# Performance work log

Hardware: AMD Instinct MI355X
Metric: run time of the kernel (lower is better)

The kernel has to match this reference:

```python
import jax, jax.numpy as jnp
import numpy as np

B, T, N_EMBED, HEAD_SIZE = 4096, 50, 600, 100
CHUNK = N_EMBED // HEAD_SIZE  # 6: per-group input channels of the grouped 1x1 conv


def _grouped_proj(x, w):
    # Conv1d(kernel=1, groups=HEAD_SIZE, bias=False): output channel h is a dot
    # product of its weight row with the h-th CHUNK-slice of the embedding.
    xr = x.reshape(x.shape[0], x.shape[1], HEAD_SIZE, CHUNK)  # [B,T,H,chunk]
    return jnp.einsum('bthc,hc->bth', xr, w)  # [B,T,HEAD_SIZE]


def setup_inputs() -> dict:
    key = jax.random.key(0)
    k0, k1, k2, k3 = jax.random.split(key, 4)
    scale = 1.0 / np.sqrt(CHUNK)
    x = jax.random.normal(k0, (B, T, N_EMBED), dtype=jnp.float32)
    w_q = jax.random.normal(k1, (HEAD_SIZE, CHUNK), dtype=jnp.float32) * scale
    w_k = jax.random.normal(k2, (HEAD_SIZE, CHUNK), dtype=jnp.float32) * scale
    w_v = jax.random.normal(k3, (HEAD_SIZE, CHUNK), dtype=jnp.float32) * scale
    return {"x": x, "w_q": w_q, "w_k": w_k, "w_v": w_v}


def reference(x, w_q, w_k, w_v):
    Bx, Tx, C = x.shape
    q = _grouped_proj(x, w_q)  # [B,T,H]
    k = _grouped_proj(x, w_k)  # [B,T,H]
    v = _grouped_proj(x, w_v)  # [B,T,H]
    # scores scaled by full embed dim C (as in the source), causal mask, softmax
    wei = jnp.einsum('bth,bsh->bts', q, k) * (C ** -0.5)  # [B,T,T]
    causal = jnp.tril(jnp.ones((Tx, Tx), dtype=bool))
    wei = jnp.where(causal, wei, -jnp.inf)
    wei = jax.nn.softmax(wei, axis=-1)
    out = jnp.einsum('bts,bsh->bth', wei, v)  # [B,T,HEAD_SIZE]
    return out
```

## Files before the change

kernel.cpp:

```cpp
#include <hip/hip_runtime.h>
#include <hip/hip_bf16.h>


#define BATCH 4096
#define TT 50
#define HH 100
#define CC 600

typedef __attribute__((ext_vector_type(8))) short short8;
typedef __attribute__((ext_vector_type(4))) short short4v;
typedef __attribute__((ext_vector_type(4))) float f32x4;
typedef unsigned short ushort_t;

constexpr int NTHR = 256;
constexpr int NWAVES = 4;
constexpr float kScale = 0.04082482904638630163f;

constexpr int OQ = 0, OKk = 6400, OV = 12800, OP = 19968, LDS_US = 24064;

__device__ __forceinline__ ushort_t f2bf(float f) {
    return __builtin_bit_cast(ushort_t, __float2bfloat16(f));
}
__device__ __forceinline__ float bf2f(ushort_t h) {
    return __uint_as_float(((unsigned)h) << 16);
}

__global__ __launch_bounds__(NTHR, 3) void headc_fused(
    const float* __restrict__ x,
    const float* __restrict__ wq,
    const float* __restrict__ wk,
    const float* __restrict__ wv,
    float* __restrict__ out)
{
    __shared__ __align__(16) ushort_t lds[LDS_US];

    const int b = blockIdx.x;
    const int tid = threadIdx.x;
    const float* xb = x + (size_t)b * (TT * CC);

    {
        const short8 z8 = {0, 0, 0, 0, 0, 0, 0, 0};
        const short4v z4 = {0, 0, 0, 0};
        if (tid < 100) {
            const int arr = tid / 50;
            const int r = tid % 50;
            const int base = (arr ? OKk : OQ) + r * 128;
            *reinterpret_cast<short4v*>(lds + base + ((12 ^ (r & 7)) << 3) + 4) = z4;
            *reinterpret_cast<short8*>(lds + base + ((13 ^ (r & 7)) << 3)) = z8;
            *reinterpret_cast<short8*>(lds + base + ((14 ^ (r & 7)) << 3)) = z8;
            *reinterpret_cast<short8*>(lds + base + ((15 ^ (r & 7)) << 3)) = z8;
            #pragma unroll
            for (int rr = 0; rr < 2; ++rr) {
                const int vr = tid + rr * 100;
                if (vr < 100) {
                    *reinterpret_cast<short4v*>(lds + OV + vr * 64 + ((6 ^ (vr & 7)) << 3) + 4) = z4;
                    *reinterpret_cast<short8*>(lds + OV + vr * 64 + ((7 ^ (vr & 7)) << 3)) = z8;
                }
            }
        } else if (tid < 196) {
            const int idx = tid - 100;
            const int r = 100 + (idx >> 3);
            const int gr = idx & 7;
            *reinterpret_cast<short8*>(lds + OV + r * 64 + gr * 8) = z8;
        } else if (tid < 246) {
            const int vr = tid - 196 + 50;
            *reinterpret_cast<short4v*>(lds + OV + vr * 64 + ((6 ^ (vr & 7)) << 3) + 4) = z4;
            *reinterpret_cast<short8*>(lds + OV + vr * 64 + ((7 ^ (vr & 7)) << 3)) = z8;
        }
    }

    if (tid < 250) {
        const int hp = tid % 50;
        const int c  = tid / 50;
        const int h0 = hp * 2;
        const float4 wqa = *(const float4*)(wq + h0 * 6);
        const float4 wqb = *(const float4*)(wq + h0 * 6 + 4);
        const float4 wqc = *(const float4*)(wq + h0 * 6 + 8);
        const float4 wka = *(const float4*)(wk + h0 * 6);
        const float4 wkb = *(const float4*)(wk + h0 * 6 + 4);
        const float4 wkc = *(const float4*)(wk + h0 * 6 + 8);
        const float4 wva = *(const float4*)(wv + h0 * 6);
        const float4 wvb = *(const float4*)(wv + h0 * 6 + 4);
        const float4 wvc = *(const float4*)(wv + h0 * 6 + 8);

        #pragma unroll
        for (int u = 0; u < 3; ++u) {
            const int qd = c + u * 5;
            if (qd <= 12) {
                const int tbase = qd * 4;
                float4 xr[4][3];
                #pragma unroll
                for (int r = 0; r < 4; ++r) {
                    const int tc = (tbase + r < TT) ? (tbase + r) : (TT - 1);
                    const float* xp = xb + tc * CC + h0 * 6;
                    xr[r][0] = *(const float4*)xp;
                    xr[r][1] = *(const float4*)(xp + 4);
                    xr[r][2] = *(const float4*)(xp + 8);
                }
                short4v vp0 = {0, 0, 0, 0};
                short4v vp1 = {0, 0, 0, 0};
                #pragma unroll
                for (int r = 0; r < 4; ++r) {
                    const int t = tbase + r;
                    const float4 xa = xr[r][0], xm = xr[r][1], xc = xr[r][2];
                    float q0 = xa.x*wqa.x + xa.y*wqa.y + xa.z*wqa.z + xa.w*wqa.w + xm.x*wqb.x + xm.y*wqb.y;
                    float q1 = xm.z*wqb.z + xm.w*wqb.w + xc.x*wqc.x + xc.y*wqc.y + xc.z*wqc.z + xc.w*wqc.w;
                    float k0 = xa.x*wka.x + xa.y*wka.y + xa.z*wka.z + xa.w*wka.w + xm.x*wkb.x + xm.y*wkb.y;
                    float k1 = xm.z*wkb.z + xm.w*wkb.w + xc.x*wkc.x + xc.y*wkc.y + xc.z*wkc.z + xc.w*wkc.w;
                    float v0 = xa.x*wva.x + xa.y*wva.y + xa.z*wva.z + xa.w*wva.w + xm.x*wvb.x + xm.y*wvb.y;
                    float v1 = xm.z*wvb.z + xm.w*wvb.w + xc.x*wvc.x + xc.y*wvc.y + xc.z*wvc.z + xc.w*wvc.w;
                    q0 *= kScale; q1 *= kScale;
                    if (t < TT) {
                        const int qg = (((h0 >> 3) ^ (t & 7)) << 3) + (h0 & 7);
                        *reinterpret_cast<unsigned*>(lds + OQ  + t * 128 + qg) =
                            (unsigned)f2bf(q0) | ((unsigned)f2bf(q1) << 16);
                        *reinterpret_cast<unsigned*>(lds + OKk + t * 128 + qg) =
                            (unsigned)f2bf(k0) | ((unsigned)f2bf(k1) << 16);
                        vp0[r] = (short)f2bf(v0);
                        vp1[r] = (short)f2bf(v1);
                    }
                }
                const int g = qd >> 1, half = (qd & 1) * 4;
                *reinterpret_cast<short4v*>(lds + OV + h0 * 64 + ((g ^ (h0 & 7)) << 3) + half) = vp0;
                *reinterpret_cast<short4v*>(lds + OV + (h0 + 1) * 64 + ((g ^ ((h0 + 1) & 7)) << 3) + half) = vp1;
            }
        }
    }
    __syncthreads();

    const int wv_ = tid >> 6;
    const int lane = tid & 63;
    const int l15 = lane & 15, l4 = lane >> 4;

    for (int p = wv_; p < 10; p += NWAVES) {
        const int tm = (p >= 6) ? 3 : (p >= 3) ? 2 : (p >= 1) ? 1 : 0;
        const int sn = p - tm * (tm + 1) / 2;
        f32x4 acc = {0.f, 0.f, 0.f, 0.f};
        const int ar = tm * 16 + l15;
        const int br = sn * 16 + l15;
        #pragma unroll
        for (int kk = 0; kk < 4; ++kk) {
            const int g = kk * 4 + l4;
            const short8 a  = *reinterpret_cast<const short8*>(lds + OQ  + ar * 128 + ((g ^ (ar & 7)) << 3));
            const short8 bb = *reinterpret_cast<const short8*>(lds + OKk + br * 128 + ((g ^ (br & 7)) << 3));
            acc = __builtin_amdgcn_mfma_f32_16x16x32_bf16(a, bb, acc, 0, 0, 0);
        }
        const int row0 = tm * 16 + l4 * 4;
        const int col = sn * 16 + l15;
        #pragma unroll
        for (int r = 0; r < 4; ++r) {
            const int row = row0 + r;
            lds[OP + row * 64 + (((col >> 3) ^ (row & 7)) << 3) + (col & 7)] = f2bf(acc[r]);
        }
    }
    __syncthreads();

    {
        const int t = tid >> 2, ll = tid & 3;
        if (t < TT) {
            const int ga = (2 * ll) ^ (t & 7), gb = (2 * ll + 1) ^ (t & 7);
            const short8 pa = *reinterpret_cast<const short8*>(lds + OP + t * 64 + (ga << 3));
            const short8 pb = *reinterpret_cast<const short8*>(lds + OP + t * 64 + (gb << 3));
            float v[16];
            float mx = -3.4e38f;
            #pragma unroll
            for (int j = 0; j < 8; ++j) {
                const int s = 16 * ll + j;
                v[j] = bf2f((ushort_t)pa[j]);
                if (s <= t) mx = fmaxf(mx, v[j]);
            }
            #pragma unroll
            for (int j = 0; j < 8; ++j) {
                const int s = 16 * ll + 8 + j;
                v[8 + j] = bf2f((ushort_t)pb[j]);
                if (s <= t) mx = fmaxf(mx, v[8 + j]);
            }
            mx = fmaxf(mx, __shfl_xor(mx, 1));
            mx = fmaxf(mx, __shfl_xor(mx, 2));
            float sum = 0.f;
            #pragma unroll
            for (int j = 0; j < 16; ++j) {
                const int s = 16 * ll + j;
                const float e = (s <= t) ? __expf(v[j] - mx) : 0.f;
                v[j] = e;
                sum += e;
            }
            sum += __shfl_xor(sum, 1);
            sum += __shfl_xor(sum, 2);
            const float inv = 1.f / sum;
            short8 wa, wb;
            #pragma unroll
            for (int j = 0; j < 8; ++j) {
                wa[j] = (short)f2bf(v[j] * inv);
                wb[j] = (short)f2bf(v[8 + j] * inv);
            }
            *reinterpret_cast<short8*>(lds + OP + t * 64 + (ga << 3)) = wa;
            *reinterpret_cast<short8*>(lds + OP + t * 64 + (gb << 3)) = wb;
        }
    }
    __syncthreads();

    float* ob = out + (size_t)b * (TT * HH);
    for (int p = wv_; p < 28; p += NWAVES) {
        const int tm = p / 7, hn = p - tm * 7;
        f32x4 acc = {0.f, 0.f, 0.f, 0.f};
        const int ar = tm * 16 + l15;
        const int br = hn * 16 + l15;
        #pragma unroll
        for (int kk = 0; kk < 2; ++kk) {
            const int g = kk * 4 + l4;
            const short8 a  = *reinterpret_cast<const short8*>(lds + OP + ar * 64 + ((g ^ (ar & 7)) << 3));
            const short8 bb = *reinterpret_cast<const short8*>(lds + OV + br * 64 + ((g ^ (br & 7)) << 3));
            acc = __builtin_amdgcn_mfma_f32_16x16x32_bf16(a, bb, acc, 0, 0, 0);
        }
        const int h = hn * 16 + l15;
        const int t0 = tm * 16 + l4 * 4;
        if (h < HH) {
            #pragma unroll
            for (int r = 0; r < 4; ++r) {
                const int t = t0 + r;
                if (t < TT) ob[t * HH + h] = acc[r];
            }
        }
    }
}

extern "C" void kernel_launch(void* const* d_in, const int* in_sizes, int n_in,
                              void* d_out, int out_size, void* d_ws, size_t ws_size,
                              hipStream_t stream) {
    const float* x  = (const float*)d_in[0];
    const float* wq = (const float*)d_in[1];
    const float* wk = (const float*)d_in[2];
    const float* wv = (const float*)d_in[3];
    float* out = (float*)d_out;
    headc_fused<<<dim3(BATCH), dim3(NTHR), 0, stream>>>(x, wq, wk, wv, out);
}
```

Measured before the change: 121.5 us.

## Process eight batches per block with double-buffered LDS and prefetched x loads

Each block now handles eight batch elements in sequence instead of one. The x loads for the next element are issued into registers before the current element's attention runs, and the projection writes into an alternate LDS buffer, so global-memory latency overlaps with MFMA and softmax work. The score matrix P reuses the other buffer's Q region. This raises register use (three x tile sets held at once) and LDS per block, lowers occupancy to two blocks per SM in launch bounds, and leaves a grid of only 512 blocks, which may not fill the device well.

```diff
diff --git a/kernel.cpp b/kernel.cpp
--- a/kernel.cpp
+++ b/kernel.cpp
@@ -14,9 +14,14 @@
 
 constexpr int NTHR = 256;
 constexpr int NWAVES = 4;
+constexpr int NB = 8;
+constexpr int GRID = BATCH / NB;
 constexpr float kScale = 0.04082482904638630163f;
 
-constexpr int OQ = 0, OKk = 6400, OV = 12800, OP = 19968, LDS_US = 24064;
+constexpr int BUF_US = 19200;
+constexpr int RQ = 0, RK = 6400, RV = 12800;
+constexpr int PAD_US = 38400;
+constexpr int LDS_US = 39168;
 
 __device__ __forceinline__ ushort_t f2bf(float f) {
     return __builtin_bit_cast(ushort_t, __float2bfloat16(f));
@@ -24,8 +29,13 @@
 __device__ __forceinline__ float bf2f(ushort_t h) {
     return __uint_as_float(((unsigned)h) << 16);
 }
-
-__global__ __launch_bounds__(NTHR, 3) void headc_fused(
+__device__ __forceinline__ void bar_lds() {
+    asm volatile("s_waitcnt lgkmcnt(0)" ::: "memory");
+    __builtin_amdgcn_s_barrier();
+    asm volatile("" ::: "memory");
+}
+
+__global__ __launch_bounds__(NTHR, 2) void headc_fused(
     const float* __restrict__ x,
     const float* __restrict__ wq,
     const float* __restrict__ wk,
@@ -34,193 +44,232 @@
 {
     __shared__ __align__(16) ushort_t lds[LDS_US];
 
-    const int b = blockIdx.x;
     const int tid = threadIdx.x;
-    const float* xb = x + (size_t)b * (TT * CC);
+    const float* xblk = x + (size_t)blockIdx.x * NB * (TT * CC);
+    float* oblk = out + (size_t)blockIdx.x * NB * (TT * HH);
+
+    const int hp = tid % 50;
+    const int c = tid / 50;
+    const int h0 = hp * 2;
+    const int nqd = (c >= 3) ? 2 : 3;
+    const bool pactive = (tid < 250);
 
     {
         const short8 z8 = {0, 0, 0, 0, 0, 0, 0, 0};
         const short4v z4 = {0, 0, 0, 0};
-        if (tid < 100) {
-            const int arr = tid / 50;
-            const int r = tid % 50;
-            const int base = (arr ? OKk : OQ) + r * 128;
-            *reinterpret_cast<short4v*>(lds + base + ((12 ^ (r & 7)) << 3) + 4) = z4;
-            *reinterpret_cast<short8*>(lds + base + ((13 ^ (r & 7)) << 3)) = z8;
-            *reinterpret_cast<short8*>(lds + base + ((14 ^ (r & 7)) << 3)) = z8;
-            *reinterpret_cast<short8*>(lds + base + ((15 ^ (r & 7)) << 3)) = z8;
-            #pragma unroll
-            for (int rr = 0; rr < 2; ++rr) {
-                const int vr = tid + rr * 100;
-                if (vr < 100) {
-                    *reinterpret_cast<short4v*>(lds + OV + vr * 64 + ((6 ^ (vr & 7)) << 3) + 4) = z4;
-                    *reinterpret_cast<short8*>(lds + OV + vr * 64 + ((7 ^ (vr & 7)) << 3)) = z8;
-                }
-            }
-        } else if (tid < 196) {
-            const int idx = tid - 100;
-            const int r = 100 + (idx >> 3);
-            const int gr = idx & 7;
-            *reinterpret_cast<short8*>(lds + OV + r * 64 + gr * 8) = z8;
-        } else if (tid < 246) {
-            const int vr = tid - 196 + 50;
-            *reinterpret_cast<short4v*>(lds + OV + vr * 64 + ((6 ^ (vr & 7)) << 3) + 4) = z4;
-            *reinterpret_cast<short8*>(lds + OV + vr * 64 + ((7 ^ (vr & 7)) << 3)) = z8;
-        }
+        for (int j = tid; j < 400; j += NTHR) {
+            if (j < 200) {
+                const int buf = (j >= 100) ? BUF_US : 0;
+                const int arr = ((j / 50) & 1) ? RK : RQ;
+                const int r = j % 50;
+                const int base = buf + arr + r * 128;
+                *reinterpret_cast<short4v*>(lds + base + ((12 ^ (r & 7)) << 3) + 4) = z4;
+                *reinterpret_cast<short8*>(lds + base + ((13 ^ (r & 7)) << 3)) = z8;
+                *reinterpret_cast<short8*>(lds + base + ((14 ^ (r & 7)) << 3)) = z8;
+                *reinterpret_cast<short8*>(lds + base + ((15 ^ (r & 7)) << 3)) = z8;
+            } else {
+                const int jj = j - 200;
+                const int buf = (jj >= 100) ? BUF_US : 0;
+                const int h = jj % 100;
+                const int base = buf + RV + h * 64;
+                *reinterpret_cast<short4v*>(lds + base + ((6 ^ (h & 7)) << 3) + 4) = z4;
+                *reinterpret_cast<short8*>(lds + base + ((7 ^ (h & 7)) << 3)) = z8;
+            }
+        }
+        for (int j = tid; j < 96; j += NTHR)
+            *reinterpret_cast<short8*>(lds + PAD_US + j * 8) = z8;
     }
 
-    if (tid < 250) {
-        const int hp = tid % 50;
-        const int c  = tid / 50;
-        const int h0 = hp * 2;
-        const float4 wqa = *(const float4*)(wq + h0 * 6);
-        const float4 wqb = *(const float4*)(wq + h0 * 6 + 4);
-        const float4 wqc = *(const float4*)(wq + h0 * 6 + 8);
-        const float4 wka = *(const float4*)(wk + h0 * 6);
-        const float4 wkb = *(const float4*)(wk + h0 * 6 + 4);
-        const float4 wkc = *(const float4*)(wk + h0 * 6 + 8);
-        const float4 wva = *(const float4*)(wv + h0 * 6);
-        const float4 wvb = *(const float4*)(wv + h0 * 6 + 4);
-        const float4 wvc = *(const float4*)(wv + h0 * 6 + 8);
-
-        #pragma unroll
-        for (int u = 0; u < 3; ++u) {
-            const int qd = c + u * 5;
-            if (qd <= 12) {
-                const int tbase = qd * 4;
-                float4 xr[4][3];
-                #pragma unroll
-                for (int r = 0; r < 4; ++r) {
-                    const int tc = (tbase + r < TT) ? (tbase + r) : (TT - 1);
-                    const float* xp = xb + tc * CC + h0 * 6;
-                    xr[r][0] = *(const float4*)xp;
-                    xr[r][1] = *(const float4*)(xp + 4);
-                    xr[r][2] = *(const float4*)(xp + 8);
-                }
-                short4v vp0 = {0, 0, 0, 0};
-                short4v vp1 = {0, 0, 0, 0};
-                #pragma unroll
-                for (int r = 0; r < 4; ++r) {
-                    const int t = tbase + r;
-                    const float4 xa = xr[r][0], xm = xr[r][1], xc = xr[r][2];
-                    float q0 = xa.x*wqa.x + xa.y*wqa.y + xa.z*wqa.z + xa.w*wqa.w + xm.x*wqb.x + xm.y*wqb.y;
-                    float q1 = xm.z*wqb.z + xm.w*wqb.w + xc.x*wqc.x + xc.y*wqc.y + xc.z*wqc.z + xc.w*wqc.w;
-                    float k0 = xa.x*wka.x + xa.y*wka.y + xa.z*wka.z + xa.w*wka.w + xm.x*wkb.x + xm.y*wkb.y;
-                    float k1 = xm.z*wkb.z + xm.w*wkb.w + xc.x*wkc.x + xc.y*wkc.y + xc.z*wkc.z + xc.w*wkc.w;
-                    float v0 = xa.x*wva.x + xa.y*wva.y + xa.z*wva.z + xa.w*wva.w + xm.x*wvb.x + xm.y*wvb.y;
-                    float v1 = xm.z*wvb.z + xm.w*wvb.w + xc.x*wvc.x + xc.y*wvc.y + xc.z*wvc.z + xc.w*wvc.w;
-                    q0 *= kScale; q1 *= kScale;
-                    if (t < TT) {
-                        const int qg = (((h0 >> 3) ^ (t & 7)) << 3) + (h0 & 7);
-                        *reinterpret_cast<unsigned*>(lds + OQ  + t * 128 + qg) =
-                            (unsigned)f2bf(q0) | ((unsigned)f2bf(q1) << 16);
-                        *reinterpret_cast<unsigned*>(lds + OKk + t * 128 + qg) =
-                            (unsigned)f2bf(k0) | ((unsigned)f2bf(k1) << 16);
-                        vp0[r] = (short)f2bf(v0);
-                        vp1[r] = (short)f2bf(v1);
+    float4 w0, w1, w2, w3, w4, w5, w6, w7, w8;
+    if (pactive) {
+        w0 = *(const float4*)(wq + h0 * 6);
+        w1 = *(const float4*)(wq + h0 * 6 + 4);
+        w2 = *(const float4*)(wq + h0 * 6 + 8);
+        w3 = *(const float4*)(wk + h0 * 6);
+        w4 = *(const float4*)(wk + h0 * 6 + 4);
+        w5 = *(const float4*)(wk + h0 * 6 + 8);
+        w6 = *(const float4*)(wv + h0 * 6);
+        w7 = *(const float4*)(wv + h0 * 6 + 4);
+        w8 = *(const float4*)(wv + h0 * 6 + 8);
+    }
+
+    float4 xr[3][4][3];
+
+    auto issue_x = [&](int bi) {
+        if (pactive) {
+            const float* xb = xblk + (size_t)bi * (TT * CC);
+            #pragma unroll
+            for (int u = 0; u < 3; ++u) {
+                if (u < nqd) {
+                    const int tb = (c + u * 5) * 4;
+                    #pragma unroll
+                    for (int r = 0; r < 4; ++r) {
+                        const int tc = (tb + r < TT) ? (tb + r) : (TT - 1);
+                        const float* xp = xb + tc * CC + h0 * 6;
+                        xr[u][r][0] = *(const float4*)xp;
+                        xr[u][r][1] = *(const float4*)(xp + 4);
+                        xr[u][r][2] = *(const float4*)(xp + 8);
                     }
                 }
-                const int g = qd >> 1, half = (qd & 1) * 4;
-                *reinterpret_cast<short4v*>(lds + OV + h0 * 64 + ((g ^ (h0 & 7)) << 3) + half) = vp0;
-                *reinterpret_cast<short4v*>(lds + OV + (h0 + 1) * 64 + ((g ^ ((h0 + 1) & 7)) << 3) + half) = vp1;
-            }
-        }
-    }
-    __syncthreads();
+            }
+        }
+    };
+
+    auto do_proj = [&](int base) {
+        if (pactive) {
+            #pragma unroll
+            for (int u = 0; u < 3; ++u) {
+                if (u < nqd) {
+                    const int qd = c + u * 5;
+                    const int tb = qd * 4;
+                    short4v vp0 = {0, 0, 0, 0}, vp1 = {0, 0, 0, 0};
+                    #pragma unroll
+                    for (int r = 0; r < 4; ++r) {
+                        const int t = tb + r;
+                        const float4 xa = xr[u][r][0], xm = xr[u][r][1], xc = xr[u][r][2];
+                        float q0 = xa.x*w0.x + xa.y*w0.y + xa.z*w0.z + xa.w*w0.w + xm.x*w1.x + xm.y*w1.y;
+                        float q1 = xm.z*w1.z + xm.w*w1.w + xc.x*w2.x + xc.y*w2.y + xc.z*w2.z + xc.w*w2.w;
+                        float k0 = xa.x*w3.x + xa.y*w3.y + xa.z*w3.z + xa.w*w3.w + xm.x*w4.x + xm.y*w4.y;
+                        float k1 = xm.z*w4.z + xm.w*w4.w + xc.x*w5.x + xc.y*w5.y + xc.z*w5.z + xc.w*w5.w;
+                        float v0 = xa.x*w6.x + xa.y*w6.y + xa.z*w6.z + xa.w*w6.w + xm.x*w7.x + xm.y*w7.y;
+                        float v1 = xm.z*w7.z + xm.w*w7.w + xc.x*w8.x + xc.y*w8.y + xc.z*w8.z + xc.w*w8.w;
+                        q0 *= kScale; q1 *= kScale;
+                        if (t < TT) {
+                            const int qg = (((h0 >> 3) ^ (t & 7)) << 3) + (h0 & 7);
+                            *reinterpret_cast<unsigned*>(lds + base + RQ + t * 128 + qg) =
+                                (unsigned)f2bf(q0) | ((unsigned)f2bf(q1) << 16);
+                            *reinterpret_cast<unsigned*>(lds + base + RK + t * 128 + qg) =
+                                (unsigned)f2bf(k0) | ((unsigned)f2bf(k1) << 16);
+                            vp0[r] = (short)f2bf(v0);
+                            vp1[r] = (short)f2bf(v1);
+                        }
+                    }
+                    const int g = qd >> 1, half = (qd & 1) * 4;
+                    *reinterpret_cast<short4v*>(lds + base + RV + h0 * 64 + ((g ^ (h0 & 7)) << 3) + half) = vp0;
+                    *reinterpret_cast<short4v*>(lds + base + RV + (h0 + 1) * 64 + ((g ^ ((h0 + 1) & 7)) << 3) + half) = vp1;
+                }
+            }
+        }
+    };
+
+    issue_x(0);
+    __builtin_amdgcn_sched_barrier(0);
+    do_proj(0);
 
     const int wv_ = tid >> 6;
     const int lane = tid & 63;
     const int l15 = lane & 15, l4 = lane >> 4;
 
-    for (int p = wv_; p < 10; p += NWAVES) {
-        const int tm = (p >= 6) ? 3 : (p >= 3) ? 2 : (p >= 1) ? 1 : 0;
-        const int sn = p - tm * (tm + 1) / 2;
-        f32x4 acc = {0.f, 0.f, 0.f, 0.f};
-        const int ar = tm * 16 + l15;
-        const int br = sn * 16 + l15;
-        #pragma unroll
-        for (int kk = 0; kk < 4; ++kk) {
-            const int g = kk * 4 + l4;
-            const short8 a  = *reinterpret_cast<const short8*>(lds + OQ  + ar * 128 + ((g ^ (ar & 7)) << 3));
-            const short8 bb = *reinterpret_cast<const short8*>(lds + OKk + br * 128 + ((g ^ (br & 7)) << 3));
-            acc = __builtin_amdgcn_mfma_f32_16x16x32_bf16(a, bb, acc, 0, 0, 0);
-        }
-        const int row0 = tm * 16 + l4 * 4;
-        const int col = sn * 16 + l15;
-        #pragma unroll
-        for (int r = 0; r < 4; ++r) {
-            const int row = row0 + r;
-            lds[OP + row * 64 + (((col >> 3) ^ (row & 7)) << 3) + (col & 7)] = f2bf(acc[r]);
-        }
-    }
-    __syncthreads();
-
-    {
-        const int t = tid >> 2, ll = tid & 3;
-        if (t < TT) {
-            const int ga = (2 * ll) ^ (t & 7), gb = (2 * ll + 1) ^ (t & 7);
-            const short8 pa = *reinterpret_cast<const short8*>(lds + OP + t * 64 + (ga << 3));
-            const short8 pb = *reinterpret_cast<const short8*>(lds + OP + t * 64 + (gb << 3));
-            float v[16];
-            float mx = -3.4e38f;
-            #pragma unroll
-            for (int j = 0; j < 8; ++j) {
-                const int s = 16 * ll + j;
-                v[j] = bf2f((ushort_t)pa[j]);
-                if (s <= t) mx = fmaxf(mx, v[j]);
-            }
-            #pragma unroll
-            for (int j = 0; j < 8; ++j) {
-                const int s = 16 * ll + 8 + j;
-                v[8 + j] = bf2f((ushort_t)pb[j]);
-                if (s <= t) mx = fmaxf(mx, v[8 + j]);
-            }
-            mx = fmaxf(mx, __shfl_xor(mx, 1));
-            mx = fmaxf(mx, __shfl_xor(mx, 2));
-            float sum = 0.f;
-            #pragma unroll
-            for (int j = 0; j < 16; ++j) {
-                const int s = 16 * ll + j;
-                const float e = (s <= t) ? __expf(v[j] - mx) : 0.f;
-                v[j] = e;
-                sum += e;
-            }
-            sum += __shfl_xor(sum, 1);
-            sum += __shfl_xor(sum, 2);
-            const float inv = 1.f / sum;
-            short8 wa, wb;
-            #pragma unroll
-            for (int j = 0; j < 8; ++j) {
-                wa[j] = (short)f2bf(v[j] * inv);
-                wb[j] = (short)f2bf(v[8 + j] * inv);
-            }
-            *reinterpret_cast<short8*>(lds + OP + t * 64 + (ga << 3)) = wa;
-            *reinterpret_cast<short8*>(lds + OP + t * 64 + (gb << 3)) = wb;
-        }
-    }
-    __syncthreads();
-
-    float* ob = out + (size_t)b * (TT * HH);
-    for (int p = wv_; p < 28; p += NWAVES) {
-        const int tm = p / 7, hn = p - tm * 7;
-        f32x4 acc = {0.f, 0.f, 0.f, 0.f};
-        const int ar = tm * 16 + l15;
-        const int br = hn * 16 + l15;
-        #pragma unroll
-        for (int kk = 0; kk < 2; ++kk) {
-            const int g = kk * 4 + l4;
-            const short8 a  = *reinterpret_cast<const short8*>(lds + OP + ar * 64 + ((g ^ (ar & 7)) << 3));
-            const short8 bb = *reinterpret_cast<const short8*>(lds + OV + br * 64 + ((g ^ (br & 7)) << 3));
-            acc = __builtin_amdgcn_mfma_f32_16x16x32_bf16(a, bb, acc, 0, 0, 0);
-        }
-        const int h = hn * 16 + l15;
-        const int t0 = tm * 16 + l4 * 4;
-        if (h < HH) {
+    #pragma unroll 2
+    for (int i = 0; i < NB; ++i) {
+        const int cur = (i & 1) * BUF_US;
+        const int oth = BUF_US - cur;
+        const int OP = oth + RQ;
+
+        if (i + 1 < NB) {
+            issue_x(i + 1);
+            __builtin_amdgcn_sched_barrier(0);
+        }
+
+        bar_lds();
+
+        for (int p = wv_; p < 10; p += NWAVES) {
+            const int tm = (p >= 6) ? 3 : (p >= 3) ? 2 : (p >= 1) ? 1 : 0;
+            const int sn = p - tm * (tm + 1) / 2;
+            f32x4 acc = {0.f, 0.f, 0.f, 0.f};
+            const int ar = tm * 16 + l15;
+            const int br = sn * 16 + l15;
+            #pragma unroll
+            for (int kk = 0; kk < 4; ++kk) {
+                const int g = kk * 4 + l4;
+                const short8 a  = *reinterpret_cast<const short8*>(lds + cur + RQ + ar * 128 + ((g ^ (ar & 7)) << 3));
+                const short8 bb = *reinterpret_cast<const short8*>(lds + cur + RK + br * 128 + ((g ^ (br & 7)) << 3));
+                acc = __builtin_amdgcn_mfma_f32_16x16x32_bf16(a, bb, acc, 0, 0, 0);
+            }
+            const int row0 = tm * 16 + l4 * 4;
+            const int col = sn * 16 + l15;
             #pragma unroll
             for (int r = 0; r < 4; ++r) {
-                const int t = t0 + r;
-                if (t < TT) ob[t * HH + h] = acc[r];
-            }
+                const int row = row0 + r;
+                lds[OP + row * 64 + (((col >> 3) ^ (row & 7)) << 3) + (col & 7)] = f2bf(acc[r]);
+            }
+        }
+        bar_lds();
+
+        {
+            const int t = tid >> 2, ll = tid & 3;
+            if (t < TT) {
+                const int ga = (2 * ll) ^ (t & 7), gb = (2 * ll + 1) ^ (t & 7);
+                const short8 pa = *reinterpret_cast<const short8*>(lds + OP + t * 64 + (ga << 3));
+                const short8 pb = *reinterpret_cast<const short8*>(lds + OP + t * 64 + (gb << 3));
+                float v[16];
+                float mx = -3.4e38f;
+                #pragma unroll
+                for (int j = 0; j < 8; ++j) {
+                    const int s = 16 * ll + j;
+                    v[j] = bf2f((ushort_t)pa[j]);
+                    if (s <= t) mx = fmaxf(mx, v[j]);
+                }
+                #pragma unroll
+                for (int j = 0; j < 8; ++j) {
+                    const int s = 16 * ll + 8 + j;
+                    v[8 + j] = bf2f((ushort_t)pb[j]);
+                    if (s <= t) mx = fmaxf(mx, v[8 + j]);
+                }
+                mx = fmaxf(mx, __shfl_xor(mx, 1));
+                mx = fmaxf(mx, __shfl_xor(mx, 2));
+                float sum = 0.f;
+                #pragma unroll
+                for (int j = 0; j < 16; ++j) {
+                    const int s = 16 * ll + j;
+                    const float e = (s <= t) ? __expf(v[j] - mx) : 0.f;
+                    v[j] = e;
+                    sum += e;
+                }
+                sum += __shfl_xor(sum, 1);
+                sum += __shfl_xor(sum, 2);
+                const float inv = 1.f / sum;
+                short8 wa, wb;
+                #pragma unroll
+                for (int j = 0; j < 8; ++j) {
+                    wa[j] = (short)f2bf(v[j] * inv);
+                    wb[j] = (short)f2bf(v[8 + j] * inv);
+                }
+                *reinterpret_cast<short8*>(lds + OP + t * 64 + (ga << 3)) = wa;
+                *reinterpret_cast<short8*>(lds + OP + t * 64 + (gb << 3)) = wb;
+            }
+        }
+        bar_lds();
+
+        {
+            float* ob = oblk + (size_t)i * (TT * HH);
+            for (int p = wv_; p < 28; p += NWAVES) {
+                const int tm = p / 7, hn = p - tm * 7;
+                f32x4 acc = {0.f, 0.f, 0.f, 0.f};
+                const int ar = tm * 16 + l15;
+                const int br = hn * 16 + l15;
+                #pragma unroll
+                for (int kk = 0; kk < 2; ++kk) {
+                    const int g = kk * 4 + l4;
+                    const short8 a  = *reinterpret_cast<const short8*>(lds + OP + ar * 64 + ((g ^ (ar & 7)) << 3));
+                    const short8 bb = *reinterpret_cast<const short8*>(lds + cur + RV + br * 64 + ((g ^ (br & 7)) << 3));
+                    acc = __builtin_amdgcn_mfma_f32_16x16x32_bf16(a, bb, acc, 0, 0, 0);
+                }
+                const int h = hn * 16 + l15;
+                const int t0 = tm * 16 + l4 * 4;
+                if (h < HH) {
+                    #pragma unroll
+                    for (int r = 0; r < 4; ++r) {
+                        const int t = t0 + r;
+                        if (t < TT) ob[t * HH + h] = acc[r];
+                    }
+                }
+            }
+        }
+
+        if (i + 1 < NB) {
+            bar_lds();
+            do_proj(oth);
         }
     }
 }
@@ -233,5 +282,5 @@
     const float* wk = (const float*)d_in[2];
     const float* wv = (const float*)d_in[3];
     float* out = (float*)d_out;
-    headc_fused<<<dim3(BATCH), dim3(NTHR), 0, stream>>>(x, wq, wk, wv, out);
-}
+    headc_fused<<<dim3(GRID), dim3(NTHR), 0, stream>>>(x, wq, wk, wv, out);
+}
```

After: 141.5 us. 16.5% more time.

## Fuse QK^T scores with softmax in registers and pipeline x loads

Applied to the files above, without the earlier changes.

Each wave now owns one 16-row query tile. It computes its causal score tiles with MFMA and runs the softmax directly on the accumulator registers, using cross-lane shuffles instead of writing the scores to LDS and reading them back. This removes the separate P buffer and one block barrier, and the normalized probabilities are written over the Q region, which shrinks LDS. The x loads for the projection are double-buffered so the next chunk is in flight while the current one is projected. The trade-off is an uneven per-wave workload across the causal triangle, and padded rows of K, P and V are read without being zeroed, relying on masking and on unstored output columns.

```diff
diff --git a/kernel.cpp b/kernel.cpp
--- a/kernel.cpp
+++ b/kernel.cpp
@@ -16,13 +16,15 @@
 constexpr int NWAVES = 4;
 constexpr float kScale = 0.04082482904638630163f;
 
-constexpr int OQ = 0, OKk = 6400, OV = 12800, OP = 19968, LDS_US = 24064;
+constexpr int RQ = 0, RK = 6400, RV = 12800, LDS_US = 19968;
 
 __device__ __forceinline__ ushort_t f2bf(float f) {
     return __builtin_bit_cast(ushort_t, __float2bfloat16(f));
 }
-__device__ __forceinline__ float bf2f(ushort_t h) {
-    return __uint_as_float(((unsigned)h) << 16);
+__device__ __forceinline__ void bar_lds() {
+    asm volatile("s_waitcnt lgkmcnt(0)" ::: "memory");
+    __builtin_amdgcn_s_barrier();
+    asm volatile("" ::: "memory");
 }
 
 __global__ __launch_bounds__(NTHR, 3) void headc_fused(
@@ -34,174 +36,168 @@
 {
     __shared__ __align__(16) ushort_t lds[LDS_US];
 
+    const int tid = threadIdx.x;
     const int b = blockIdx.x;
-    const int tid = threadIdx.x;
     const float* xb = x + (size_t)b * (TT * CC);
 
     {
         const short8 z8 = {0, 0, 0, 0, 0, 0, 0, 0};
         const short4v z4 = {0, 0, 0, 0};
-        if (tid < 100) {
-            const int arr = tid / 50;
-            const int r = tid % 50;
-            const int base = (arr ? OKk : OQ) + r * 128;
-            *reinterpret_cast<short4v*>(lds + base + ((12 ^ (r & 7)) << 3) + 4) = z4;
-            *reinterpret_cast<short8*>(lds + base + ((13 ^ (r & 7)) << 3)) = z8;
-            *reinterpret_cast<short8*>(lds + base + ((14 ^ (r & 7)) << 3)) = z8;
-            *reinterpret_cast<short8*>(lds + base + ((15 ^ (r & 7)) << 3)) = z8;
-            #pragma unroll
-            for (int rr = 0; rr < 2; ++rr) {
-                const int vr = tid + rr * 100;
-                if (vr < 100) {
-                    *reinterpret_cast<short4v*>(lds + OV + vr * 64 + ((6 ^ (vr & 7)) << 3) + 4) = z4;
-                    *reinterpret_cast<short8*>(lds + OV + vr * 64 + ((7 ^ (vr & 7)) << 3)) = z8;
+        if (tid < 200) {
+            if (tid < 100) {
+                const int arr = tid / 50;
+                const int r = tid % 50;
+                const int base = (arr ? RK : RQ) + r * 128;
+                *reinterpret_cast<short4v*>(lds + base + ((12 ^ (r & 7)) << 3) + 4) = z4;
+                *reinterpret_cast<short8*>(lds + base + ((13 ^ (r & 7)) << 3)) = z8;
+                *reinterpret_cast<short8*>(lds + base + ((14 ^ (r & 7)) << 3)) = z8;
+                *reinterpret_cast<short8*>(lds + base + ((15 ^ (r & 7)) << 3)) = z8;
+            } else {
+                const int h = tid - 100;
+                const int base = RV + h * 64;
+                *reinterpret_cast<short4v*>(lds + base + ((6 ^ (h & 7)) << 3) + 4) = z4;
+                *reinterpret_cast<short8*>(lds + base + ((7 ^ (h & 7)) << 3)) = z8;
+            }
+        }
+    }
+
+    const int hp = tid % 50;
+    const int c = tid / 50;
+    const int h0 = hp * 2;
+    const bool pactive = (tid < 250);
+    const bool has3 = (c < 3);
+
+    if (pactive) {
+        const float4 w0 = *(const float4*)(wq + h0 * 6);
+        const float4 w1 = *(const float4*)(wq + h0 * 6 + 4);
+        const float4 w2 = *(const float4*)(wq + h0 * 6 + 8);
+        const float4 w3 = *(const float4*)(wk + h0 * 6);
+        const float4 w4 = *(const float4*)(wk + h0 * 6 + 4);
+        const float4 w5 = *(const float4*)(wk + h0 * 6 + 8);
+        const float4 w6 = *(const float4*)(wv + h0 * 6);
+        const float4 w7 = *(const float4*)(wv + h0 * 6 + 4);
+        const float4 w8 = *(const float4*)(wv + h0 * 6 + 8);
+
+        float4 xA[4][3], xB[4][3];
+
+        auto issue = [&](float4 (&xr)[4][3], int qd) {
+            const int tb = qd * 4;
+            #pragma unroll
+            for (int r = 0; r < 4; ++r) {
+                const int tc = (tb + r < TT) ? (tb + r) : (TT - 1);
+                const float* xp = xb + tc * CC + h0 * 6;
+                xr[r][0] = *(const float4*)xp;
+                xr[r][1] = *(const float4*)(xp + 4);
+                xr[r][2] = *(const float4*)(xp + 8);
+            }
+        };
+        auto proj = [&](const float4 (&xr)[4][3], int qd) {
+            const int tb = qd * 4;
+            short4v vp0 = {0, 0, 0, 0}, vp1 = {0, 0, 0, 0};
+            #pragma unroll
+            for (int r = 0; r < 4; ++r) {
+                const int t = tb + r;
+                const float4 xa = xr[r][0], xm = xr[r][1], xc = xr[r][2];
+                float q0 = xa.x*w0.x + xa.y*w0.y + xa.z*w0.z + xa.w*w0.w + xm.x*w1.x + xm.y*w1.y;
+                float q1 = xm.z*w1.z + xm.w*w1.w + xc.x*w2.x + xc.y*w2.y + xc.z*w2.z + xc.w*w2.w;
+                float k0 = xa.x*w3.x + xa.y*w3.y + xa.z*w3.z + xa.w*w3.w + xm.x*w4.x + xm.y*w4.y;
+                float k1 = xm.z*w4.z + xm.w*w4.w + xc.x*w5.x + xc.y*w5.y + xc.z*w5.z + xc.w*w5.w;
+                float v0 = xa.x*w6.x + xa.y*w6.y + xa.z*w6.z + xa.w*w6.w + xm.x*w7.x + xm.y*w7.y;
+                float v1 = xm.z*w7.z + xm.w*w7.w + xc.x*w8.x + xc.y*w8.y + xc.z*w8.z + xc.w*w8.w;
+                q0 *= kScale; q1 *= kScale;
+                if (t < TT) {
+                    const int qg = (((h0 >> 3) ^ (t & 7)) << 3) + (h0 & 7);
+                    *reinterpret_cast<unsigned*>(lds + RQ + t * 128 + qg) =
+                        (unsigned)f2bf(q0) | ((unsigned)f2bf(q1) << 16);
+                    *reinterpret_cast<unsigned*>(lds + RK + t * 128 + qg) =
+                        (unsigned)f2bf(k0) | ((unsigned)f2bf(k1) << 16);
+                    vp0[r] = (short)f2bf(v0);
+                    vp1[r] = (short)f2bf(v1);
                 }
             }
-        } else if (tid < 196) {
-            const int idx = tid - 100;
-            const int r = 100 + (idx >> 3);
-            const int gr = idx & 7;
-            *reinterpret_cast<short8*>(lds + OV + r * 64 + gr * 8) = z8;
-        } else if (tid < 246) {
-            const int vr = tid - 196 + 50;
-            *reinterpret_cast<short4v*>(lds + OV + vr * 64 + ((6 ^ (vr & 7)) << 3) + 4) = z4;
-            *reinterpret_cast<short8*>(lds + OV + vr * 64 + ((7 ^ (vr & 7)) << 3)) = z8;
-        }
-    }
-
-    if (tid < 250) {
-        const int hp = tid % 50;
-        const int c  = tid / 50;
-        const int h0 = hp * 2;
-        const float4 wqa = *(const float4*)(wq + h0 * 6);
-        const float4 wqb = *(const float4*)(wq + h0 * 6 + 4);
-        const float4 wqc = *(const float4*)(wq + h0 * 6 + 8);
-        const float4 wka = *(const float4*)(wk + h0 * 6);
-        const float4 wkb = *(const float4*)(wk + h0 * 6 + 4);
-        const float4 wkc = *(const float4*)(wk + h0 * 6 + 8);
-        const float4 wva = *(const float4*)(wv + h0 * 6);
-        const float4 wvb = *(const float4*)(wv + h0 * 6 + 4);
-        const float4 wvc = *(const float4*)(wv + h0 * 6 + 8);
-
-        #pragma unroll
-        for (int u = 0; u < 3; ++u) {
-            const int qd = c + u * 5;
-            if (qd <= 12) {
-                const int tbase = qd * 4;
-                float4 xr[4][3];
-                #pragma unroll
-                for (int r = 0; r < 4; ++r) {
-                    const int tc = (tbase + r < TT) ? (tbase + r) : (TT - 1);
-                    const float* xp = xb + tc * CC + h0 * 6;
-                    xr[r][0] = *(const float4*)xp;
-                    xr[r][1] = *(const float4*)(xp + 4);
-                    xr[r][2] = *(const float4*)(xp + 8);
-                }
-                short4v vp0 = {0, 0, 0, 0};
-                short4v vp1 = {0, 0, 0, 0};
-                #pragma unroll
-                for (int r = 0; r < 4; ++r) {
-                    const int t = tbase + r;
-                    const float4 xa = xr[r][0], xm = xr[r][1], xc = xr[r][2];
-                    float q0 = xa.x*wqa.x + xa.y*wqa.y + xa.z*wqa.z + xa.w*wqa.w + xm.x*wqb.x + xm.y*wqb.y;
-                    float q1 = xm.z*wqb.z + xm.w*wqb.w + xc.x*wqc.x + xc.y*wqc.y + xc.z*wqc.z + xc.w*wqc.w;
-                    float k0 = xa.x*wka.x + xa.y*wka.y + xa.z*wka.z + xa.w*wka.w + xm.x*wkb.x + xm.y*wkb.y;
-                    float k1 = xm.z*wkb.z + xm.w*wkb.w + xc.x*wkc.x + xc.y*wkc.y + xc.z*wkc.z + xc.w*wkc.w;
-                    float v0 = xa.x*wva.x + xa.y*wva.y + xa.z*wva.z + xa.w*wva.w + xm.x*wvb.x + xm.y*wvb.y;
-                    float v1 = xm.z*wvb.z + xm.w*wvb.w + xc.x*wvc.x + xc.y*wvc.y + xc.z*wvc.z + xc.w*wvc.w;
-                    q0 *= kScale; q1 *= kScale;
-                    if (t < TT) {
-                        const int qg = (((h0 >> 3) ^ (t & 7)) << 3) + (h0 & 7);
-                        *reinterpret_cast<unsigned*>(lds + OQ  + t * 128 + qg) =
-                            (unsigned)f2bf(q0) | ((unsigned)f2bf(q1) << 16);
-                        *reinterpret_cast<unsigned*>(lds + OKk + t * 128 + qg) =
-                            (unsigned)f2bf(k0) | ((unsigned)f2bf(k1) << 16);
-                        vp0[r] = (short)f2bf(v0);
-                        vp1[r] = (short)f2bf(v1);
-                    }
-                }
-                const int g = qd >> 1, half = (qd & 1) * 4;
-                *reinterpret_cast<short4v*>(lds + OV + h0 * 64 + ((g ^ (h0 & 7)) << 3) + half) = vp0;
-                *reinterpret_cast<short4v*>(lds + OV + (h0 + 1) * 64 + ((g ^ ((h0 + 1) & 7)) << 3) + half) = vp1;
-            }
-        }
-    }
-    __syncthreads();
-
-    const int wv_ = tid >> 6;
+            const int g = qd >> 1, half = (qd & 1) * 4;
+            *reinterpret_cast<short4v*>(lds + RV + h0 * 64 + ((g ^ (h0 & 7)) << 3) + half) = vp0;
+            *reinterpret_cast<short4v*>(lds + RV + (h0 + 1) * 64 + ((g ^ ((h0 + 1) & 7)) << 3) + half) = vp1;
+        };
+
+        issue(xA, c);
+        issue(xB, c + 5);
+        proj(xA, c);
+        if (has3) issue(xA, c + 10);
+        proj(xB, c + 5);
+        if (has3) proj(xA, c + 10);
+    }
+    bar_lds();
+
+    const int w = tid >> 6;
     const int lane = tid & 63;
     const int l15 = lane & 15, l4 = lane >> 4;
-
-    for (int p = wv_; p < 10; p += NWAVES) {
-        const int tm = (p >= 6) ? 3 : (p >= 3) ? 2 : (p >= 1) ? 1 : 0;
-        const int sn = p - tm * (tm + 1) / 2;
-        f32x4 acc = {0.f, 0.f, 0.f, 0.f};
-        const int ar = tm * 16 + l15;
-        const int br = sn * 16 + l15;
-        #pragma unroll
-        for (int kk = 0; kk < 4; ++kk) {
-            const int g = kk * 4 + l4;
-            const short8 a  = *reinterpret_cast<const short8*>(lds + OQ  + ar * 128 + ((g ^ (ar & 7)) << 3));
-            const short8 bb = *reinterpret_cast<const short8*>(lds + OKk + br * 128 + ((g ^ (br & 7)) << 3));
-            acc = __builtin_amdgcn_mfma_f32_16x16x32_bf16(a, bb, acc, 0, 0, 0);
-        }
-        const int row0 = tm * 16 + l4 * 4;
-        const int col = sn * 16 + l15;
-        #pragma unroll
-        for (int r = 0; r < 4; ++r) {
-            const int row = row0 + r;
-            lds[OP + row * 64 + (((col >> 3) ^ (row & 7)) << 3) + (col & 7)] = f2bf(acc[r]);
-        }
-    }
-    __syncthreads();
+    const int t = w * 16 + l15;
 
     {
-        const int t = tid >> 2, ll = tid & 3;
+        short8 qf[4];
+        #pragma unroll
+        for (int kk = 0; kk < 4; ++kk)
+            qf[kk] = *reinterpret_cast<const short8*>(lds + RQ + t * 128 + (((kk * 4 + l4) ^ (t & 7)) << 3));
+
+        f32x4 sacc[4];
+        #pragma unroll
+        for (int sm = 0; sm < 4; ++sm) {
+            f32x4 a = {0.f, 0.f, 0.f, 0.f};
+            if (sm <= w) {
+                const int ar = sm * 16 + l15;
+                #pragma unroll
+                for (int kk = 0; kk < 4; ++kk) {
+                    const short8 kf = *reinterpret_cast<const short8*>(lds + RK + ar * 128 + (((kk * 4 + l4) ^ (ar & 7)) << 3));
+                    a = __builtin_amdgcn_mfma_f32_16x16x32_bf16(kf, qf[kk], a, 0, 0, 0);
+                }
+            }
+            sacc[sm] = a;
+        }
+
+        float mx = -3.4e38f;
+        #pragma unroll
+        for (int sm = 0; sm < 4; ++sm) {
+            #pragma unroll
+            for (int r = 0; r < 4; ++r) {
+                const int s = sm * 16 + l4 * 4 + r;
+                if (sm <= w && s <= t) mx = fmaxf(mx, sacc[sm][r]);
+            }
+        }
+        mx = fmaxf(mx, __shfl_xor(mx, 16));
+        mx = fmaxf(mx, __shfl_xor(mx, 32));
+        float sum = 0.f;
+        #pragma unroll
+        for (int sm = 0; sm < 4; ++sm) {
+            #pragma unroll
+            for (int r = 0; r < 4; ++r) {
+                const int s = sm * 16 + l4 * 4 + r;
+                const float e = (sm <= w && s <= t) ? __expf(sacc[sm][r] - mx) : 0.f;
+                sacc[sm][r] = e;
+                sum += e;
+            }
+        }
+        sum += __shfl_xor(sum, 16);
+        sum += __shfl_xor(sum, 32);
+        const float inv = 1.f / sum;
+
         if (t < TT) {
-            const int ga = (2 * ll) ^ (t & 7), gb = (2 * ll + 1) ^ (t & 7);
-            const short8 pa = *reinterpret_cast<const short8*>(lds + OP + t * 64 + (ga << 3));
-            const short8 pb = *reinterpret_cast<const short8*>(lds + OP + t * 64 + (gb << 3));
-            float v[16];
-            float mx = -3.4e38f;
-            #pragma unroll
-            for (int j = 0; j < 8; ++j) {
-                const int s = 16 * ll + j;
-                v[j] = bf2f((ushort_t)pa[j]);
-                if (s <= t) mx = fmaxf(mx, v[j]);
-            }
-            #pragma unroll
-            for (int j = 0; j < 8; ++j) {
-                const int s = 16 * ll + 8 + j;
-                v[8 + j] = bf2f((ushort_t)pb[j]);
-                if (s <= t) mx = fmaxf(mx, v[8 + j]);
-            }
-            mx = fmaxf(mx, __shfl_xor(mx, 1));
-            mx = fmaxf(mx, __shfl_xor(mx, 2));
-            float sum = 0.f;
-            #pragma unroll
-            for (int j = 0; j < 16; ++j) {
-                const int s = 16 * ll + j;
-                const float e = (s <= t) ? __expf(v[j] - mx) : 0.f;
-                v[j] = e;
-                sum += e;
-            }
-            sum += __shfl_xor(sum, 1);
-            sum += __shfl_xor(sum, 2);
-            const float inv = 1.f / sum;
-            short8 wa, wb;
-            #pragma unroll
-            for (int j = 0; j < 8; ++j) {
-                wa[j] = (short)f2bf(v[j] * inv);
-                wb[j] = (short)f2bf(v[8 + j] * inv);
-            }
-            *reinterpret_cast<short8*>(lds + OP + t * 64 + (ga << 3)) = wa;
-            *reinterpret_cast<short8*>(lds + OP + t * 64 + (gb << 3)) = wb;
-        }
-    }
-    __syncthreads();
+            #pragma unroll
+            for (int sm = 0; sm < 4; ++sm) {
+                #pragma unroll
+                for (int rp = 0; rp < 2; ++rp) {
+                    const int s0 = sm * 16 + l4 * 4 + 2 * rp;
+                    const unsigned pk = (unsigned)f2bf(sacc[sm][2 * rp] * inv)
+                                      | ((unsigned)f2bf(sacc[sm][2 * rp + 1] * inv) << 16);
+                    *reinterpret_cast<unsigned*>(lds + RQ + t * 128 + (((s0 >> 3) ^ (t & 7)) << 3) + (s0 & 7)) = pk;
+                }
+            }
+        }
+    }
+    bar_lds();
 
     float* ob = out + (size_t)b * (TT * HH);
-    for (int p = wv_; p < 28; p += NWAVES) {
+    for (int p = w; p < 28; p += NWAVES) {
         const int tm = p / 7, hn = p - tm * 7;
         f32x4 acc = {0.f, 0.f, 0.f, 0.f};
         const int ar = tm * 16 + l15;
@@ -209,8 +205,8 @@
         #pragma unroll
         for (int kk = 0; kk < 2; ++kk) {
             const int g = kk * 4 + l4;
-            const short8 a  = *reinterpret_cast<const short8*>(lds + OP + ar * 64 + ((g ^ (ar & 7)) << 3));
-            const short8 bb = *reinterpret_cast<const short8*>(lds + OV + br * 64 + ((g ^ (br & 7)) << 3));
+            const short8 a  = *reinterpret_cast<const short8*>(lds + RQ + ar * 128 + ((g ^ (ar & 7)) << 3));
+            const short8 bb = *reinterpret_cast<const short8*>(lds + RV + br * 64 + ((g ^ (br & 7)) << 3));
             acc = __builtin_amdgcn_mfma_f32_16x16x32_bf16(a, bb, acc, 0, 0, 0);
         }
         const int h = hn * 16 + l15;
@@ -218,8 +214,8 @@
         if (h < HH) {
             #pragma unroll
             for (int r = 0; r < 4; ++r) {
-                const int t = t0 + r;
-                if (t < TT) ob[t * HH + h] = acc[r];
+                const int tt = t0 + r;
+                if (tt < TT) ob[tt * HH + h] = acc[r];
             }
         }
     }
```

Measured after the change: 121.3 us. About the same (-0.2%).
